# Kernel optimization log

Hardware: AMD Instinct MI355X
Metric: run time of the kernel (lower is better)

Reference implementation:

```python
import jax, jax.numpy as jnp
import numpy as np

B, S, D = 4, 2048, 1024
H = 16
HD = D // H  # head_dim = 64


def setup_inputs() -> dict:
    key = jax.random.key(0)
    ks = jax.random.split(key, 5)
    scale = 1.0 / np.sqrt(D)
    return {
        "sequence_features": jax.random.normal(ks[0], (B, S, D), dtype=jnp.float32),
        "Wq": jax.random.normal(ks[1], (D, D), dtype=jnp.float32) * scale,
        "bq": jnp.zeros((D,), dtype=jnp.float32),
        "Wk": jax.random.normal(ks[2], (D, D), dtype=jnp.float32) * scale,
        "bk": jnp.zeros((D,), dtype=jnp.float32),
        "Wv": jax.random.normal(ks[3], (D, D), dtype=jnp.float32) * scale,
        "bv": jnp.zeros((D,), dtype=jnp.float32),
        "Wo": jax.random.normal(ks[4], (D, D), dtype=jnp.float32) * scale,
        "bo": jnp.zeros((D,), dtype=jnp.float32),
    }


def reference(sequence_features, Wq, bq, Wk, bk, Wv, bv, Wo, bo):
    x = sequence_features  # [B, S, D]
    # projections (torch Linear: x @ W.T + b; here W stored as [D_in, D_out])
    Q = x @ Wq + bq
    K = x @ Wk + bk
    V = x @ Wv + bv
    # split heads -> [B, H, S, HD]
    def heads(t):
        return t.reshape(B, S, H, HD).transpose(0, 2, 1, 3)
    Qh, Kh, Vh = heads(Q), heads(K), heads(V)
    # scaled dot-product attention (no mask, dropout off / eval mode)
    energy = jnp.einsum("bhqd,bhkd->bhqk", Qh, Kh) / jnp.sqrt(jnp.float32(HD))
    attn = jax.nn.softmax(energy, axis=-1)
    ctx = jnp.einsum("bhqk,bhkd->bhqd", attn, Vh)  # [B, H, S, HD]
    ctx = ctx.transpose(0, 2, 1, 3).reshape(B, S, D)
    out = ctx @ Wo + bo  # [B, S, D]
    return out.mean(axis=1)  # context vector [B, D]
```

## Files before the change

kernel.cpp:

```cpp
#include <hip/hip_runtime.h>
#include <hip/hip_bf16.h>

#define NB 4
#define NS 2048
#define ND 1024
#define NH 16

typedef __attribute__((ext_vector_type(8))) short short8;
typedef __attribute__((ext_vector_type(4))) float f32x4;
typedef __attribute__((ext_vector_type(16))) float f32x16;
typedef __attribute__((ext_vector_type(2))) int v2i;

__device__ __forceinline__ unsigned short f2b(float f) {
  unsigned int u = __float_as_uint(f);
  u = (u + 0x7fffu + ((u >> 16) & 1u)) >> 16;
  return (unsigned short)u;
}
__device__ __forceinline__ unsigned int pkbf(float a, float b) {
  return (unsigned int)f2b(a) | ((unsigned int)f2b(b) << 16);
}
__device__ __forceinline__ unsigned int cvtpk(float lo, float hi) {
  unsigned int r;
  asm("v_cvt_pk_bf16_f32 %0, %1, %2" : "=v"(r) : "v"(lo), "v"(hi));
  return r;
}
__device__ __forceinline__ v2i plswap(unsigned int a, unsigned int b) {
  return __builtin_amdgcn_permlane32_swap((int)a, (int)b, false, false);
}
__device__ __forceinline__ void gload16(const void* g, void* l) {
  __builtin_amdgcn_global_load_lds(
      (const __attribute__((address_space(1))) unsigned int*)g,
      (__attribute__((address_space(3))) unsigned int*)l, 16, 0, 0);
}
__device__ __forceinline__ int sw2(int row) { return (row ^ (row >> 2)) & 3; }

__global__ void conv_x(const float* __restrict__ x, unsigned short* __restrict__ xb) {
  int i = blockIdx.x * 256 + threadIdx.x;
  float4 v = ((const float4*)x)[i];
  ushort4 o;
  o.x = f2b(v.x); o.y = f2b(v.y); o.z = f2b(v.z); o.w = f2b(v.w);
  ((ushort4*)xb)[i] = o;
}

__global__ void conv_wt(const float* __restrict__ Wq, const float* __restrict__ Wk,
                        const float* __restrict__ Wv, unsigned short* __restrict__ Wtq,
                        unsigned short* __restrict__ Wtk, unsigned short* __restrict__ Wtv) {
  const int z = blockIdx.z;
  const float* W = (z == 0) ? Wq : (z == 1) ? Wk : Wv;
  unsigned short* Wt = (z == 0) ? Wtq : (z == 1) ? Wtk : Wtv;
  __shared__ float t[32][33];
  const int tid = threadIdx.x;
  const int row = tid >> 3, c4 = (tid & 7) * 4;
  float4 v = *(const float4*)(W + (size_t)(blockIdx.y * 32 + row) * ND + blockIdx.x * 32 + c4);
  t[row][c4] = v.x; t[row][c4 + 1] = v.y; t[row][c4 + 2] = v.z; t[row][c4 + 3] = v.w;
  __syncthreads();
  ushort4 o;
  o.x = f2b(t[c4][row]); o.y = f2b(t[c4 + 1][row]);
  o.z = f2b(t[c4 + 2][row]); o.w = f2b(t[c4 + 3][row]);
  *(ushort4*)(Wt + (size_t)(blockIdx.x * 32 + row) * ND + blockIdx.y * 32 + c4) = o;
}

__global__ __launch_bounds__(256) void qkv_gemm(
    const unsigned short* __restrict__ xb,
    const unsigned short* __restrict__ Wtq, const unsigned short* __restrict__ Wtk,
    const unsigned short* __restrict__ Wtv,
    const float* __restrict__ bq, const float* __restrict__ bk, const float* __restrict__ bv,
    unsigned short* __restrict__ Qb, unsigned short* __restrict__ Kb,
    unsigned short* __restrict__ Vt) {
  const int z = blockIdx.z;
  const unsigned short* Wt = (z == 0) ? Wtq : (z == 1) ? Wtk : Wtv;
  const float* bias = (z == 0) ? bq : (z == 1) ? bk : bv;
  const int tn = blockIdx.x, tm = blockIdx.y;
  __shared__ __align__(16) unsigned short Al[2][128 * 32];
  __shared__ __align__(16) unsigned short Bl[2][128 * 32];
  const int tid = threadIdx.x;
  const int lane = tid & 63, w = tid >> 6;
  const int c = lane & 15, g = lane >> 4;
  const int mo = (w >> 1) * 64, no = (w & 1) * 64;

  f32x4 acc[4][4];
#pragma unroll
  for (int i = 0; i < 4; i++)
#pragma unroll
    for (int j = 0; j < 4; j++) acc[i][j] = (f32x4){0.f, 0.f, 0.f, 0.f};

  const int r0 = tid >> 2, g0 = tid & 3;
  const int r1 = (256 + tid) >> 2, g1 = (256 + tid) & 3;
  const unsigned short* gA0 = xb + (size_t)(tm * 128 + r0) * ND + (g0 ^ sw2(r0)) * 8;
  const unsigned short* gA1 = xb + (size_t)(tm * 128 + r1) * ND + (g1 ^ sw2(r1)) * 8;
  const unsigned short* gB0 = Wt + (size_t)(tn * 128 + r0) * ND + (g0 ^ sw2(r0)) * 8;
  const unsigned short* gB1 = Wt + (size_t)(tn * 128 + r1) * ND + (g1 ^ sw2(r1)) * 8;
  const int lo0 = w * 512, lo1 = 2048 + w * 512;

  gload16(gA0, &Al[0][lo0]); gload16(gA1, &Al[0][lo1]);
  gload16(gB0, &Bl[0][lo0]); gload16(gB1, &Bl[0][lo1]);
  __syncthreads();

  for (int kk = 0; kk < 32; ++kk) {
    const int cur = kk & 1;
    if (kk < 31) {
      const int ko = (kk + 1) * 32;
      gload16(gA0 + ko, &Al[cur ^ 1][lo0]); gload16(gA1 + ko, &Al[cur ^ 1][lo1]);
      gload16(gB0 + ko, &Bl[cur ^ 1][lo0]); gload16(gB1 + ko, &Bl[cur ^ 1][lo1]);
    }
    short8 af[4], bf[4];
#pragma unroll
    for (int i = 0; i < 4; i++) {
      int row = mo + i * 16 + c;
      af[i] = *(const short8*)&Al[cur][row * 32 + (g ^ sw2(row)) * 8];
    }
#pragma unroll
    for (int j = 0; j < 4; j++) {
      int row = no + j * 16 + c;
      bf[j] = *(const short8*)&Bl[cur][row * 32 + (g ^ sw2(row)) * 8];
    }
#pragma unroll
    for (int i = 0; i < 4; i++)
#pragma unroll
      for (int j = 0; j < 4; j++)
        acc[i][j] = __builtin_amdgcn_mfma_f32_16x16x32_bf16(af[i], bf[j], acc[i][j], 0, 0, 0);
    __syncthreads();
  }

  if (z < 2) {
    unsigned short* Out = (z == 0) ? Qb : Kb;
    const float sc = (z == 0) ? 0.125f : 1.0f;
#pragma unroll
    for (int j = 0; j < 4; j++) {
      int col = tn * 128 + no + j * 16 + c;
      float bv_ = bias[col];
#pragma unroll
      for (int i = 0; i < 4; i++) {
        int rowb = tm * 128 + mo + i * 16 + 4 * g;
#pragma unroll
        for (int r = 0; r < 4; r++) {
          float v = (acc[i][j][r] + bv_) * sc;
          float vn = __shfl_xor(v, 1, 64);
          if (!(lane & 1))
            *(unsigned int*)(Out + (size_t)(rowb + r) * ND + col) = pkbf(v, vn);
        }
      }
    }
  } else {
#pragma unroll
    for (int j = 0; j < 4; j++) {
      int col = tn * 128 + no + j * 16 + c;
      float bv_ = bias[col];
      int h = col >> 6, hd = col & 63;
#pragma unroll
      for (int i = 0; i < 4; i++) {
        int rowg = tm * 128 + mo + i * 16 + 4 * g;
        int bi = rowg >> 11, s = rowg & 2047;
        uint2 u;
        u.x = pkbf(acc[i][j][0] + bv_, acc[i][j][1] + bv_);
        u.y = pkbf(acc[i][j][2] + bv_, acc[i][j][3] + bv_);
        *(uint2*)(Vt + ((size_t)((bi * NH + h) * 64 + hd) * NS + s)) = u;
      }
    }
  }
}

__device__ __forceinline__ void softmax_pack(const f32x16& e, float& m, float& l,
                                             f32x16& c0, f32x16& c1, int hi,
                                             short8* pa) {
  float pm = e[0];
#pragma unroll
  for (int r = 1; r < 16; r++) pm = fmaxf(pm, e[r]);
  pm = fmaxf(pm, __shfl_xor(pm, 32, 64));
  if (__any(pm > m + 8.f)) {
    float mn = fmaxf(m, pm);
    float sf = __expf(m - mn);
#pragma unroll
    for (int r = 0; r < 16; r++) {
      int qlr = (r & 3) + 8 * (r >> 2) + 4 * hi;
      float sr = __shfl(sf, qlr, 64);
      c0[r] *= sr; c1[r] *= sr;
    }
    l *= sf; m = mn;
  }
  float p[16];
#pragma unroll
  for (int r = 0; r < 16; r++) p[r] = __expf(e[r] - m);
  float cs = 0.f;
#pragma unroll
  for (int r = 0; r < 16; r++) cs += p[r];
  cs += __shfl_xor(cs, 32, 64);
  l += cs;
  unsigned int u0[4], u1[4];
#pragma unroll
  for (int mq = 0; mq < 4; mq++) {
    u0[mq] = cvtpk(p[4 * mq], p[4 * mq + 1]);
    u1[mq] = cvtpk(p[4 * mq + 2], p[4 * mq + 3]);
  }
#pragma unroll
  for (int si = 0; si < 2; si++) {
    v2i a = plswap(u0[2 * si], u0[2 * si + 1]);
    v2i bb = plswap(u1[2 * si], u1[2 * si + 1]);
    union { unsigned int u[4]; short8 v; } pf;
    pf.u[0] = (unsigned int)a[0];
    pf.u[1] = (unsigned int)bb[0];
    pf.u[2] = (unsigned int)a[1];
    pf.u[3] = (unsigned int)bb[1];
    pa[si] = pf.v;
  }
}

__global__ __launch_bounds__(256) void attn_kernel(
    const unsigned short* __restrict__ Qb, const unsigned short* __restrict__ Kb,
    const unsigned short* __restrict__ Vt, float* __restrict__ mean_part) {
  const int qt = blockIdx.x, h = blockIdx.y, b = blockIdx.z;
  const int tid = threadIdx.x, lane = tid & 63, w = tid >> 6;
  const int ql_ = lane & 31, hi = lane >> 5;

  __shared__ __align__(16) unsigned short Kl[2][64 * 64];
  __shared__ __align__(16) unsigned short Vl[2][64 * 64];
  __shared__ float redl[4][64];

  short8 qf[2][4];
#pragma unroll
  for (int qg = 0; qg < 2; qg++) {
    const unsigned short* qb =
        Qb + ((size_t)b * NS + qt * 256 + w * 64 + qg * 32 + ql_) * ND + h * 64 + 8 * hi;
#pragma unroll
    for (int s = 0; s < 4; s++) qf[qg][s] = *(const short8*)(qb + 16 * s);
  }

  const int rid = tid >> 3, gcol = tid & 7;
  const int gsw = (gcol ^ (rid & 7)) * 8;
  const unsigned short* gK0 = Kb + ((size_t)b * NS + rid) * ND + h * 64 + gsw;
  const unsigned short* gK1 = gK0 + (size_t)32 * ND;
  const unsigned short* gV0 = Vt + ((size_t)(b * NH + h) * 64 + rid) * NS + gsw;
  const unsigned short* gV1 = gV0 + (size_t)32 * NS;

#define STAGE_KV(buf, kc)                                              \
  {                                                                    \
    const size_t ko = (size_t)(kc) * 64;                               \
    gload16(gK0 + ko * ND, &Kl[buf][w * 512]);                         \
    gload16(gK1 + ko * ND, &Kl[buf][2048 + w * 512]);                  \
    gload16(gV0 + ko, &Vl[buf][w * 512]);                              \
    gload16(gV1 + ko, &Vl[buf][2048 + w * 512]);                       \
  }

  const f32x16 Z16 = {0.f, 0.f, 0.f, 0.f, 0.f, 0.f, 0.f, 0.f,
                      0.f, 0.f, 0.f, 0.f, 0.f, 0.f, 0.f, 0.f};
  f32x16 ctx00 = Z16, ctx01 = Z16, ctx10 = Z16, ctx11 = Z16;
  float m0 = -1e30f, m1 = -1e30f, l0 = 0.f, l1 = 0.f;

  STAGE_KV(0, 0);
  __syncthreads();

  for (int kc = 0; kc < 32; ++kc) {
    const int cur = kc & 1;
    if (kc < 31) STAGE_KV(cur ^ 1, kc + 1);
#pragma unroll
    for (int kg = 0; kg < 2; kg++) {
      short8 kf[4];
#pragma unroll
      for (int s = 0; s < 4; s++)
        kf[s] = *(const short8*)&Kl[cur][(kg * 32 + ql_) * 64 +
                                         (((2 * s + hi) ^ (ql_ & 7)) * 8)];
      __builtin_amdgcn_s_setprio(1);
      f32x16 e0 = __builtin_amdgcn_mfma_f32_32x32x16_bf16(kf[0], qf[0][0], Z16, 0, 0, 0);
      f32x16 e1 = __builtin_amdgcn_mfma_f32_32x32x16_bf16(kf[0], qf[1][0], Z16, 0, 0, 0);
#pragma unroll
      for (int s = 1; s < 4; s++) {
        e0 = __builtin_amdgcn_mfma_f32_32x32x16_bf16(kf[s], qf[0][s], e0, 0, 0, 0);
        e1 = __builtin_amdgcn_mfma_f32_32x32x16_bf16(kf[s], qf[1][s], e1, 0, 0, 0);
      }
      __builtin_amdgcn_s_setprio(0);

      short8 pa0[2], pa1[2];
      softmax_pack(e0, m0, l0, ctx00, ctx01, hi, pa0);
      softmax_pack(e1, m1, l1, ctx10, ctx11, hi, pa1);

      __builtin_amdgcn_s_setprio(1);
#pragma unroll
      for (int si = 0; si < 2; si++) {
#pragma unroll
        for (int dg = 0; dg < 2; dg++) {
          short8 vf = *(const short8*)&Vl[cur][(dg * 32 + ql_) * 64 +
                        (((4 * kg + 2 * si + hi) ^ (ql_ & 7)) * 8)];
          if (dg == 0) {
            ctx00 = __builtin_amdgcn_mfma_f32_32x32x16_bf16(pa0[si], vf, ctx00, 0, 0, 0);
            ctx10 = __builtin_amdgcn_mfma_f32_32x32x16_bf16(pa1[si], vf, ctx10, 0, 0, 0);
          } else {
            ctx01 = __builtin_amdgcn_mfma_f32_32x32x16_bf16(pa0[si], vf, ctx01, 0, 0, 0);
            ctx11 = __builtin_amdgcn_mfma_f32_32x32x16_bf16(pa1[si], vf, ctx11, 0, 0, 0);
          }
        }
      }
      __builtin_amdgcn_s_setprio(0);
    }
    __syncthreads();
  }

  float linv0 = 1.f / l0, linv1 = 1.f / l1;
  float s0 = 0.f, s1 = 0.f;
#pragma unroll
  for (int r = 0; r < 16; r++) {
    int qlr = (r & 3) + 8 * (r >> 2) + 4 * hi;
    float lv0 = __shfl(linv0, qlr, 64);
    float lv1 = __shfl(linv1, qlr, 64);
    s0 += ctx00[r] * lv0 + ctx10[r] * lv1;
    s1 += ctx01[r] * lv0 + ctx11[r] * lv1;
  }
  s0 += __shfl_xor(s0, 32, 64);
  s1 += __shfl_xor(s1, 32, 64);
  if (lane < 32) { redl[w][lane] = s0; redl[w][32 + lane] = s1; }
  __syncthreads();
  if (tid < 64) {
    float tot = redl[0][tid] + redl[1][tid] + redl[2][tid] + redl[3][tid];
    mean_part[((size_t)qt * NB + b) * ND + h * 64 + tid] = tot * (1.0f / (float)NS);
  }
}

__global__ void reduce_mctx(const float* __restrict__ mp, float* __restrict__ mctx) {
  int i = blockIdx.x * 256 + threadIdx.x;
  float s = 0.f;
#pragma unroll
  for (int q = 0; q < NS / 256; ++q) s += mp[(size_t)q * NB * ND + i];
  mctx[i] = s;
}

__global__ void out_proj(const float* __restrict__ mc, const float* __restrict__ Wo,
                         const float* __restrict__ bo, float* __restrict__ out) {
  const int b = blockIdx.y;
  const int d = blockIdx.x * 256 + threadIdx.x;
  const float* m = mc + (size_t)b * ND;
  float acc = bo[d];
#pragma unroll 8
  for (int k = 0; k < ND; ++k) acc = fmaf(m[k], Wo[(size_t)k * ND + d], acc);
  out[(size_t)b * ND + d] = acc;
}

extern "C" void kernel_launch(void* const* d_in, const int* in_sizes, int n_in,
                              void* d_out, int out_size, void* d_ws, size_t ws_size,
                              hipStream_t stream) {
  const float* x  = (const float*)d_in[0];
  const float* Wq = (const float*)d_in[1];
  const float* bq = (const float*)d_in[2];
  const float* Wk = (const float*)d_in[3];
  const float* bk = (const float*)d_in[4];
  const float* Wv = (const float*)d_in[5];
  const float* bv = (const float*)d_in[6];
  const float* Wo = (const float*)d_in[7];
  const float* bo = (const float*)d_in[8];
  float* out = (float*)d_out;

  char* ws = (char*)d_ws;
  size_t off = 0;
  unsigned short* xb  = (unsigned short*)(ws + off); off += (size_t)NB * NS * ND * 2;
  unsigned short* Wtq = (unsigned short*)(ws + off); off += (size_t)ND * ND * 2;
  unsigned short* Wtk = (unsigned short*)(ws + off); off += (size_t)ND * ND * 2;
  unsigned short* Wtv = (unsigned short*)(ws + off); off += (size_t)ND * ND * 2;
  unsigned short* Qb  = (unsigned short*)(ws + off); off += (size_t)NB * NS * ND * 2;
  unsigned short* Kb  = (unsigned short*)(ws + off); off += (size_t)NB * NS * ND * 2;
  unsigned short* Vt  = (unsigned short*)(ws + off); off += (size_t)NB * NS * ND * 2;
  float* mpart = (float*)(ws + off); off += (size_t)(NS / 256) * NB * ND * 4;
  float* mctx  = (float*)(ws + off); off += (size_t)NB * ND * 4;

  conv_x<<<(NB * NS * ND / 4) / 256, 256, 0, stream>>>(x, xb);
  conv_wt<<<dim3(32, 32, 3), 256, 0, stream>>>(Wq, Wk, Wv, Wtq, Wtk, Wtv);
  qkv_gemm<<<dim3(ND / 128, NB * NS / 128, 3), 256, 0, stream>>>(
      xb, Wtq, Wtk, Wtv, bq, bk, bv, Qb, Kb, Vt);
  attn_kernel<<<dim3(NS / 256, NH, NB), 256, 0, stream>>>(Qb, Kb, Vt, mpart);
  reduce_mctx<<<(NB * ND) / 256, 256, 0, stream>>>(mpart, mctx);
  out_proj<<<dim3(ND / 256, NB), 256, 0, stream>>>(mctx, Wo, bo, out);
}
```

Measured before the change: 403.1 us.

## Halve attention query tile to 128 rows per block for more blocks and occupancy

Each attention block now handles 128 queries (32 per wave) instead of 256, doubling the grid to 1024 blocks and halving per-wave accumulator registers. Launch bounds request 4 blocks per CU so the compiler limits registers. The partial mean buffer and reduction are resized for 16 query tiles. The cost is that K/V tiles are loaded from global memory twice as often per query, and each wave now issues fewer MFMAs to hide each softmax step.

```diff
diff --git a/kernel.cpp b/kernel.cpp
--- a/kernel.cpp
+++ b/kernel.cpp
@@ -205,7 +205,7 @@
   }
 }
 
-__global__ __launch_bounds__(256) void attn_kernel(
+__global__ __launch_bounds__(256, 4) void attn_kernel(
     const unsigned short* __restrict__ Qb, const unsigned short* __restrict__ Kb,
     const unsigned short* __restrict__ Vt, float* __restrict__ mean_part) {
   const int qt = blockIdx.x, h = blockIdx.y, b = blockIdx.z;
@@ -216,14 +216,11 @@
   __shared__ __align__(16) unsigned short Vl[2][64 * 64];
   __shared__ float redl[4][64];
 
-  short8 qf[2][4];
-#pragma unroll
-  for (int qg = 0; qg < 2; qg++) {
-    const unsigned short* qb =
-        Qb + ((size_t)b * NS + qt * 256 + w * 64 + qg * 32 + ql_) * ND + h * 64 + 8 * hi;
-#pragma unroll
-    for (int s = 0; s < 4; s++) qf[qg][s] = *(const short8*)(qb + 16 * s);
-  }
+  const unsigned short* qb =
+      Qb + ((size_t)b * NS + qt * 128 + w * 32 + ql_) * ND + h * 64 + 8 * hi;
+  short8 qf[4];
+#pragma unroll
+  for (int s = 0; s < 4; s++) qf[s] = *(const short8*)(qb + 16 * s);
 
   const int rid = tid >> 3, gcol = tid & 7;
   const int gsw = (gcol ^ (rid & 7)) * 8;
@@ -243,8 +240,8 @@
 
   const f32x16 Z16 = {0.f, 0.f, 0.f, 0.f, 0.f, 0.f, 0.f, 0.f,
                       0.f, 0.f, 0.f, 0.f, 0.f, 0.f, 0.f, 0.f};
-  f32x16 ctx00 = Z16, ctx01 = Z16, ctx10 = Z16, ctx11 = Z16;
-  float m0 = -1e30f, m1 = -1e30f, l0 = 0.f, l1 = 0.f;
+  f32x16 ctx0 = Z16, ctx1 = Z16;
+  float m0 = -1e30f, l0 = 0.f;
 
   STAGE_KV(0, 0);
   __syncthreads();
@@ -260,18 +257,14 @@
         kf[s] = *(const short8*)&Kl[cur][(kg * 32 + ql_) * 64 +
                                          (((2 * s + hi) ^ (ql_ & 7)) * 8)];
       __builtin_amdgcn_s_setprio(1);
-      f32x16 e0 = __builtin_amdgcn_mfma_f32_32x32x16_bf16(kf[0], qf[0][0], Z16, 0, 0, 0);
-      f32x16 e1 = __builtin_amdgcn_mfma_f32_32x32x16_bf16(kf[0], qf[1][0], Z16, 0, 0, 0);
-#pragma unroll
-      for (int s = 1; s < 4; s++) {
-        e0 = __builtin_amdgcn_mfma_f32_32x32x16_bf16(kf[s], qf[0][s], e0, 0, 0, 0);
-        e1 = __builtin_amdgcn_mfma_f32_32x32x16_bf16(kf[s], qf[1][s], e1, 0, 0, 0);
-      }
+      f32x16 e = __builtin_amdgcn_mfma_f32_32x32x16_bf16(kf[0], qf[0], Z16, 0, 0, 0);
+#pragma unroll
+      for (int s = 1; s < 4; s++)
+        e = __builtin_amdgcn_mfma_f32_32x32x16_bf16(kf[s], qf[s], e, 0, 0, 0);
       __builtin_amdgcn_s_setprio(0);
 
-      short8 pa0[2], pa1[2];
-      softmax_pack(e0, m0, l0, ctx00, ctx01, hi, pa0);
-      softmax_pack(e1, m1, l1, ctx10, ctx11, hi, pa1);
+      short8 pa[2];
+      softmax_pack(e, m0, l0, ctx0, ctx1, hi, pa);
 
       __builtin_amdgcn_s_setprio(1);
 #pragma unroll
@@ -280,13 +273,10 @@
         for (int dg = 0; dg < 2; dg++) {
           short8 vf = *(const short8*)&Vl[cur][(dg * 32 + ql_) * 64 +
                         (((4 * kg + 2 * si + hi) ^ (ql_ & 7)) * 8)];
-          if (dg == 0) {
-            ctx00 = __builtin_amdgcn_mfma_f32_32x32x16_bf16(pa0[si], vf, ctx00, 0, 0, 0);
-            ctx10 = __builtin_amdgcn_mfma_f32_32x32x16_bf16(pa1[si], vf, ctx10, 0, 0, 0);
-          } else {
-            ctx01 = __builtin_amdgcn_mfma_f32_32x32x16_bf16(pa0[si], vf, ctx01, 0, 0, 0);
-            ctx11 = __builtin_amdgcn_mfma_f32_32x32x16_bf16(pa1[si], vf, ctx11, 0, 0, 0);
-          }
+          if (dg == 0)
+            ctx0 = __builtin_amdgcn_mfma_f32_32x32x16_bf16(pa[si], vf, ctx0, 0, 0, 0);
+          else
+            ctx1 = __builtin_amdgcn_mfma_f32_32x32x16_bf16(pa[si], vf, ctx1, 0, 0, 0);
         }
       }
       __builtin_amdgcn_s_setprio(0);
@@ -294,15 +284,14 @@
     __syncthreads();
   }
 
-  float linv0 = 1.f / l0, linv1 = 1.f / l1;
+  float linv = 1.f / l0;
   float s0 = 0.f, s1 = 0.f;
 #pragma unroll
   for (int r = 0; r < 16; r++) {
     int qlr = (r & 3) + 8 * (r >> 2) + 4 * hi;
-    float lv0 = __shfl(linv0, qlr, 64);
-    float lv1 = __shfl(linv1, qlr, 64);
-    s0 += ctx00[r] * lv0 + ctx10[r] * lv1;
-    s1 += ctx01[r] * lv0 + ctx11[r] * lv1;
+    float lv = __shfl(linv, qlr, 64);
+    s0 += ctx0[r] * lv;
+    s1 += ctx1[r] * lv;
   }
   s0 += __shfl_xor(s0, 32, 64);
   s1 += __shfl_xor(s1, 32, 64);
@@ -318,7 +307,7 @@
   int i = blockIdx.x * 256 + threadIdx.x;
   float s = 0.f;
 #pragma unroll
-  for (int q = 0; q < NS / 256; ++q) s += mp[(size_t)q * NB * ND + i];
+  for (int q = 0; q < NS / 128; ++q) s += mp[(size_t)q * NB * ND + i];
   mctx[i] = s;
 }
 
@@ -356,14 +345,14 @@
   unsigned short* Qb  = (unsigned short*)(ws + off); off += (size_t)NB * NS * ND * 2;
   unsigned short* Kb  = (unsigned short*)(ws + off); off += (size_t)NB * NS * ND * 2;
   unsigned short* Vt  = (unsigned short*)(ws + off); off += (size_t)NB * NS * ND * 2;
-  float* mpart = (float*)(ws + off); off += (size_t)(NS / 256) * NB * ND * 4;
+  float* mpart = (float*)(ws + off); off += (size_t)(NS / 128) * NB * ND * 4;
   float* mctx  = (float*)(ws + off); off += (size_t)NB * ND * 4;
 
   conv_x<<<(NB * NS * ND / 4) / 256, 256, 0, stream>>>(x, xb);
   conv_wt<<<dim3(32, 32, 3), 256, 0, stream>>>(Wq, Wk, Wv, Wtq, Wtk, Wtv);
   qkv_gemm<<<dim3(ND / 128, NB * NS / 128, 3), 256, 0, stream>>>(
       xb, Wtq, Wtk, Wtv, bq, bk, bv, Qb, Kb, Vt);
-  attn_kernel<<<dim3(NS / 256, NH, NB), 256, 0, stream>>>(Qb, Kb, Vt, mpart);
+  attn_kernel<<<dim3(NS / 128, NH, NB), 256, 0, stream>>>(Qb, Kb, Vt, mpart);
   reduce_mctx<<<(NB * ND) / 256, 256, 0, stream>>>(mpart, mctx);
   out_proj<<<dim3(ND / 256, NB), 256, 0, stream>>>(mctx, Wo, bo, out);
 }
```

Measured after the change: 354.5 us. 12.1% less time.
